# Kernel tuning notes

Measured on AMD Instinct MI355X. Metric: run time of the kernel, lower is better.

## Reference

```python
import jax, jax.numpy as jnp
import numpy as np

H, W, N, B = 64, 64, 512, 32


def setup_inputs() -> dict:
    key = jax.random.key(0)
    k1, _ = jax.random.split(key)
    data = jax.random.normal(k1, (B, N, 8), dtype=jnp.float32)
    opacity = jnp.ones((N, 1), dtype=jnp.float32)
    return {"data": data, "opacity": opacity}


def reference(data, opacity):
    # data: (B, N, 8) -> image (B, 3, H, W)
    xy = jnp.tanh(data[..., :2])                       # (B,N,2) in [-1,1]
    scale = jnp.abs(data[..., 2:4]) + 0.3              # (B,N,2)
    theta = jax.nn.sigmoid(data[..., 4]) * (2.0 * np.pi)  # (B,N)
    color = data[..., 5:8]                             # (B,N,3)

    # NDC -> pixel coords (GaussianImage convention)
    px = 0.5 * ((xy[..., 0] + 1.0) * W - 1.0)          # (B,N)
    py = 0.5 * ((xy[..., 1] + 1.0) * H - 1.0)

    # 2D covariance: R diag(s^2) R^T
    c, s = jnp.cos(theta), jnp.sin(theta)
    s0sq, s1sq = scale[..., 0] ** 2, scale[..., 1] ** 2
    cov_a = c * c * s0sq + s * s * s1sq                # (B,N)
    cov_b = c * s * (s0sq - s1sq)
    cov_c = s * s * s0sq + c * c * s1sq
    det = cov_a * cov_c - cov_b * cov_b
    # conic = inverse covariance
    con_a = cov_c / det
    con_b = -cov_b / det
    con_c = cov_a / det

    xs = jnp.arange(W, dtype=jnp.float32)              # pixel x coords
    ys = jnp.arange(H, dtype=jnp.float32)
    dx = xs[None, None, :] - px[..., None]             # (B,N,W)
    dy = ys[None, None, :] - py[..., None]             # (B,N,H)

    # sigma = 0.5*(A dx^2 + C dy^2) + B dx dy  -> (B,N,H,W)
    sigma = (0.5 * con_a[..., None, None] * (dx[:, :, None, :] ** 2)
             + 0.5 * con_c[..., None, None] * (dy[:, :, :, None] ** 2)
             + con_b[..., None, None] * dy[:, :, :, None] * dx[:, :, None, :])
    alpha = opacity[None, :, 0, None, None] * jnp.exp(-sigma)  # (B,N,H,W)

    # sum blending: out[b,c,h,w] = sum_n alpha[b,n,h,w] * color[b,n,c]
    img = jnp.einsum('bnhw,bnc->bchw', alpha, color)
    return img
```

## Files before the change

### kernel.cpp

```cpp
#include <hip/hip_runtime.h>
#include <math.h>

#define Hh 64
#define Ww 64
#define Nn 512
#define Bb 32
#define NPIX (Hh * Ww)
#define TCUT 16.0f

#define L2E 1.4426950408889634f

__device__ __forceinline__ float fast_sigmoid(float x) {
    float e = __builtin_amdgcn_exp2f(-x * L2E);
    return __builtin_amdgcn_rcpf(1.0f + e);
}
__device__ __forceinline__ float fast_tanh(float x) {
    float e = __builtin_amdgcn_exp2f(x * (-2.0f * L2E));
    return fmaf(2.0f, __builtin_amdgcn_rcpf(1.0f + e), -1.0f);
}

__global__ __launch_bounds__(256) void gs_fused(const float* __restrict__ data,
                                                const float* __restrict__ opacity,
                                                float* __restrict__ out) {
    __shared__ float4 sA[Nn];
    __shared__ float4 sB[Nn];
    __shared__ float  sC[Nn];
    __shared__ float4 sD[Nn];
    __shared__ short  slist[4][Nn / 4];
    __shared__ float  comb[3][3][64];

    int bid  = blockIdx.x;
    int tile = bid & 63;
    int b    = bid >> 6;
    int t    = threadIdx.x;
    int base = b * Nn;

#pragma unroll
    for (int j = 0; j < Nn / 256; ++j) {
        int n = j * 256 + t;
        const float4* dp = (const float4*)(data) + (size_t)(base + n) * 2;
        float4 d0 = dp[0];
        float4 d1 = dp[1];

        float xy0 = fast_tanh(d0.x);
        float xy1 = fast_tanh(d0.y);
        float s0 = fabsf(d0.z) + 0.3f;
        float s1 = fabsf(d0.w) + 0.3f;
        float u  = fast_sigmoid(d1.x);
        float c  = __builtin_amdgcn_cosf(u);
        float s  = __builtin_amdgcn_sinf(u);

        float px = 0.5f * ((xy0 + 1.0f) * (float)Ww - 1.0f);
        float py = 0.5f * ((xy1 + 1.0f) * (float)Hh - 1.0f);

        float s0sq = s0 * s0, s1sq = s1 * s1;
        float cov_a = c * c * s0sq + s * s * s1sq;
        float cov_b = c * s * (s0sq - s1sq);
        float cov_c = s * s * s0sq + c * c * s1sq;
        float det = cov_a * cov_c - cov_b * cov_b;
        float inv = __builtin_amdgcn_rcpf(det);
        float con_a = cov_c * inv;
        float con_b = -cov_b * inv;
        float con_c = cov_a * inv;

        float a2 = -0.5f * con_a * L2E;
        float b2 = -con_b * L2E;
        float c2 = -0.5f * con_c * L2E;

        float q1 = -(2.0f * a2 * px + b2 * py);
        float q2 = -(2.0f * c2 * py + b2 * px);
        float q0 = a2 * px * px + b2 * px * py + c2 * py * py;

        float det2 = 4.0f * a2 * c2 - b2 * b2;
        float rinv = __builtin_amdgcn_rcpf(det2);
        float xext = __builtin_amdgcn_sqrtf(fmaxf(4.0f * TCUT * (-c2) * rinv, 0.0f));
        float yext = __builtin_amdgcn_sqrtf(fmaxf(4.0f * TCUT * (-a2) * rinv, 0.0f));

        float op = opacity[n];

        sA[n] = make_float4(q0, q1, q2, a2);
        sB[n] = make_float4(b2, c2, op * d1.y, op * d1.z);
        sC[n] = op * d1.w;
        sD[n] = make_float4(px, py, xext, yext);
    }
    __syncthreads();

    int w    = t >> 6;
    int lane = t & 63;
    int tx0  = (tile & 7) * 8;
    int ty0  = (tile >> 3) * 8;
    float fxq0 = (float)tx0, fxq1 = (float)(tx0 + 7);
    float fyq0 = (float)ty0, fyq1 = (float)(ty0 + 7);

    short* wl = slist[w];
    int cnt = 0;
#pragma unroll
    for (int r = 0; r < 2; ++r) {
        int ln = w * 128 + r * 64 + lane;
        float4 D = sD[ln];
        bool keep = (D.x + D.z >= fxq0) && (D.x - D.z <= fxq1) &&
                    (D.y + D.w >= fyq0) && (D.y - D.w <= fyq1);
        unsigned long long m = __ballot(keep);
        int pos = (int)__popcll(m & ((1ull << lane) - 1ull));
        if (keep) wl[cnt + pos] = (short)ln;
        cnt += (int)__popcll(m);
    }

    float fx = (float)(tx0 + (lane & 7));
    float fy = (float)(ty0 + (lane >> 3));
    float fx2 = fx * fx;
    float fxy = fx * fy;
    float fy2 = fy * fy;

    float accr = 0.0f, accg = 0.0f, accb = 0.0f;
#pragma unroll 4
    for (int i = 0; i < cnt; ++i) {
        int ln = wl[i];
        float4 A  = sA[ln];
        float4 Bv = sB[ln];
        float  ob = sC[ln];
        float sgm = fmaf(A.y, fx, A.x);
        sgm = fmaf(A.z, fy, sgm);
        sgm = fmaf(A.w, fx2, sgm);
        sgm = fmaf(Bv.x, fxy, sgm);
        sgm = fmaf(Bv.y, fy2, sgm);
        float e = __builtin_amdgcn_exp2f(sgm);
        accr = fmaf(e, Bv.z, accr);
        accg = fmaf(e, Bv.w, accg);
        accb = fmaf(e, ob, accb);
    }

    if (w > 0) {
        comb[w - 1][0][lane] = accr;
        comb[w - 1][1][lane] = accg;
        comb[w - 1][2][lane] = accb;
    }
    __syncthreads();
    if (w == 0) {
        accr += comb[0][0][lane] + comb[1][0][lane] + comb[2][0][lane];
        accg += comb[0][1][lane] + comb[1][1][lane] + comb[2][1][lane];
        accb += comb[0][2][lane] + comb[1][2][lane] + comb[2][2][lane];
        int pix = (ty0 + (lane >> 3)) * Ww + tx0 + (lane & 7);
        size_t obase = (size_t)b * 3 * NPIX + (size_t)pix;
        out[obase]            = accr;
        out[obase + NPIX]     = accg;
        out[obase + 2 * NPIX] = accb;
    }
}

extern "C" void kernel_launch(void* const* d_in, const int* in_sizes, int n_in,
                              void* d_out, int out_size, void* d_ws, size_t ws_size,
                              hipStream_t stream) {
    const float* data    = (const float*)d_in[0];
    const float* opacity = (const float*)d_in[1];
    float* out = (float*)d_out;

    gs_fused<<<Bb * 64, 256, 0, stream>>>(data, opacity, out);
}
```

Baseline: 12.29 us.

## Process two pixel tiles per block to halve Gaussian preprocessing redundancy

Each block now has 512 threads and covers two 8x8 tiles instead of one, so the per-Gaussian preprocessing (tanh, sigmoid, sin/cos, conic) is computed once per pair of tiles. Every thread handles exactly one Gaussian, and the four-wave culling and reduction scheme is duplicated per tile. This halves the redundant setup work and the global loads per batch image. In exchange each block is larger, there are half as many blocks, and a tile's waves may wait on the other tile at the shared barrier.

```diff
diff --git a/kernel.cpp b/kernel.cpp
--- a/kernel.cpp
+++ b/kernel.cpp
@@ -19,25 +19,24 @@
     return fmaf(2.0f, __builtin_amdgcn_rcpf(1.0f + e), -1.0f);
 }
 
-__global__ __launch_bounds__(256) void gs_fused(const float* __restrict__ data,
-                                                const float* __restrict__ opacity,
-                                                float* __restrict__ out) {
+__global__ __launch_bounds__(512, 8) void gs_fused(const float* __restrict__ data,
+                                                   const float* __restrict__ opacity,
+                                                   float* __restrict__ out) {
     __shared__ float4 sA[Nn];
     __shared__ float4 sB[Nn];
     __shared__ float  sC[Nn];
     __shared__ float4 sD[Nn];
-    __shared__ short  slist[4][Nn / 4];
-    __shared__ float  comb[3][3][64];
+    __shared__ short  slist[8][Nn / 4];
+    __shared__ float  comb[2][3][3][64];
 
-    int bid  = blockIdx.x;
-    int tile = bid & 63;
-    int b    = bid >> 6;
-    int t    = threadIdx.x;
+    int bid = blockIdx.x;
+    int tp  = bid & 31;
+    int b   = bid >> 5;
+    int t   = threadIdx.x;
     int base = b * Nn;
 
-#pragma unroll
-    for (int j = 0; j < Nn / 256; ++j) {
-        int n = j * 256 + t;
+    {
+        int n = t;
         const float4* dp = (const float4*)(data) + (size_t)(base + n) * 2;
         float4 d0 = dp[0];
         float4 d1 = dp[1];
@@ -85,10 +84,13 @@
     }
     __syncthreads();
 
-    int w    = t >> 6;
-    int lane = t & 63;
-    int tx0  = (tile & 7) * 8;
-    int ty0  = (tile >> 3) * 8;
+    int w        = t >> 6;
+    int lane     = t & 63;
+    int tile_sel = w >> 2;
+    int q        = w & 3;
+    int tile     = (tp << 1) | tile_sel;
+    int tx0      = (tile & 7) * 8;
+    int ty0      = (tile >> 3) * 8;
     float fxq0 = (float)tx0, fxq1 = (float)(tx0 + 7);
     float fyq0 = (float)ty0, fyq1 = (float)(ty0 + 7);
 
@@ -96,7 +98,7 @@
     int cnt = 0;
 #pragma unroll
     for (int r = 0; r < 2; ++r) {
-        int ln = w * 128 + r * 64 + lane;
+        int ln = q * 128 + r * 64 + lane;
         float4 D = sD[ln];
         bool keep = (D.x + D.z >= fxq0) && (D.x - D.z <= fxq1) &&
                     (D.y + D.w >= fyq0) && (D.y - D.w <= fyq1);
@@ -130,16 +132,16 @@
         accb = fmaf(e, ob, accb);
     }
 
-    if (w > 0) {
-        comb[w - 1][0][lane] = accr;
-        comb[w - 1][1][lane] = accg;
-        comb[w - 1][2][lane] = accb;
+    if (q > 0) {
+        comb[tile_sel][q - 1][0][lane] = accr;
+        comb[tile_sel][q - 1][1][lane] = accg;
+        comb[tile_sel][q - 1][2][lane] = accb;
     }
     __syncthreads();
-    if (w == 0) {
-        accr += comb[0][0][lane] + comb[1][0][lane] + comb[2][0][lane];
-        accg += comb[0][1][lane] + comb[1][1][lane] + comb[2][1][lane];
-        accb += comb[0][2][lane] + comb[1][2][lane] + comb[2][2][lane];
+    if (q == 0) {
+        accr += comb[tile_sel][0][0][lane] + comb[tile_sel][1][0][lane] + comb[tile_sel][2][0][lane];
+        accg += comb[tile_sel][0][1][lane] + comb[tile_sel][1][1][lane] + comb[tile_sel][2][1][lane];
+        accb += comb[tile_sel][0][2][lane] + comb[tile_sel][1][2][lane] + comb[tile_sel][2][2][lane];
         int pix = (ty0 + (lane >> 3)) * Ww + tx0 + (lane & 7);
         size_t obase = (size_t)b * 3 * NPIX + (size_t)pix;
         out[obase]            = accr;
@@ -155,5 +157,5 @@
     const float* opacity = (const float*)d_in[1];
     float* out = (float*)d_out;
 
-    gs_fused<<<Bb * 64, 256, 0, stream>>>(data, opacity, out);
+    gs_fused<<<Bb * 32, 512, 0, stream>>>(data, opacity, out);
 }
```

After: 10.84 us. 11.9% less time.
